# Kernel tuning notes

Measured on AMD Instinct MI355X. Metric: run time of the kernel, lower is better.

Reference implementation:

```python
import jax, jax.numpy as jnp
import numpy as np

T, B, D_IN, D_H, D_MID, D_OUT = 16, 16384, 64, 256, 64, 4


def setup_inputs() -> dict:
    key = jax.random.key(0)
    ks = jax.random.split(key, 12)
    s = 0.05
    return {
        "x": jax.random.normal(ks[0], (T, B, D_IN), dtype=jnp.float32),
        "hc1": jnp.zeros((B, D_H), dtype=jnp.float32),
        "W_i2h": jax.random.normal(ks[1], (D_H, D_IN), dtype=jnp.float32) * s,
        "b_i2h": jax.random.normal(ks[2], (D_H,), dtype=jnp.float32) * s,
        "W_h2h": jax.random.normal(ks[3], (D_H, D_H), dtype=jnp.float32) * s,
        "b_h2h": jax.random.normal(ks[4], (D_H,), dtype=jnp.float32) * s,
        "W_h2o": jax.random.normal(ks[5], (D_MID, D_H), dtype=jnp.float32) * s,
        "b_h2o": jax.random.normal(ks[6], (D_MID,), dtype=jnp.float32) * s,
        "W_fc": jax.random.normal(ks[7], (D_OUT, D_MID), dtype=jnp.float32) * s,
        "b_fc": jax.random.normal(ks[8], (D_OUT,), dtype=jnp.float32) * s,
    }


def reference(x, hc1, W_i2h, b_i2h, W_h2h, b_h2h, W_h2o, b_h2o, W_fc, b_fc):
    # 16-step vanilla RNN: h = tanh(i2h(x_t) + h2h(h)); out = fc(tanh(h2o(h)))
    def step(h, xt):
        h_new = jnp.tanh(xt @ W_i2h.T + b_i2h + h @ W_h2h.T + b_h2h)  # [B, 256]
        out = jnp.tanh(h_new @ W_h2o.T + b_h2o) @ W_fc.T + b_fc       # [B, 4]
        return h_new, out

    h_final, output_seq = jax.lax.scan(step, hc1, x)
    return output_seq, h_final
```

## Files before the change

kernel.cpp:

```cpp
#include <hip/hip_runtime.h>


typedef _Float16 half8 __attribute__((ext_vector_type(8)));
typedef float floatx4 __attribute__((ext_vector_type(4)));

#define T_STEPS 16
#define BATCH   16384
#define HS      264
#define MS      72

__device__ inline float fast_tanh(float x) {
    float t = __builtin_amdgcn_exp2f(x * 2.8853900817779268f);
    return 1.0f - 2.0f * __builtin_amdgcn_rcpf(t + 1.0f);
}

__device__ inline half8 cvt8(const float* __restrict__ p) {
    float4 a = ((const float4*)p)[0];
    float4 b = ((const float4*)p)[1];
    half8 h;
    h[0] = (_Float16)a.x; h[1] = (_Float16)a.y; h[2] = (_Float16)a.z; h[3] = (_Float16)a.w;
    h[4] = (_Float16)b.x; h[5] = (_Float16)b.y; h[6] = (_Float16)b.z; h[7] = (_Float16)b.w;
    return h;
}

__global__ __launch_bounds__(256, 1) void rnn_kernel(
    const float* __restrict__ x,   const float* __restrict__ hc1,
    const float* __restrict__ Wi,  const float* __restrict__ bi,
    const float* __restrict__ Wh,  const float* __restrict__ bh,
    const float* __restrict__ Wo,  const float* __restrict__ bo,
    const float* __restrict__ Wf,  const float* __restrict__ bf,
    float* __restrict__ out)
{
    __shared__ _Float16 h_lds[64 * HS];
    __shared__ _Float16 mid_lds[64 * MS];
    __shared__ float    biasPre[256];
    __shared__ float    bo_lds[64];
    __shared__ _Float16 wfc_lds[4 * 64];
    __shared__ float    bfc_lds[4];

    const int tid  = threadIdx.x;
    const int w    = tid >> 6;
    const int lane = tid & 63;
    const int l16  = lane & 15;
    const int quad = lane >> 4;
    const int b0   = blockIdx.x * 64;

    biasPre[tid] = bi[tid] + bh[tid];
    if (tid < 64) bo_lds[tid] = bo[tid];
    wfc_lds[tid] = (_Float16)Wf[tid];
    if (tid < 4) bfc_lds[tid] = bf[tid];

    {
        int r = tid >> 2, c0 = (tid & 3) * 64;
        const float4* src = (const float4*)&hc1[(size_t)(b0 + r) * 256 + c0];
        #pragma unroll
        for (int i = 0; i < 16; ++i) {
            float4 v = src[i];
            int c = c0 + i * 4;
            h_lds[r * HS + c + 0] = (_Float16)v.x;
            h_lds[r * HS + c + 1] = (_Float16)v.y;
            h_lds[r * HS + c + 2] = (_Float16)v.z;
            h_lds[r * HS + c + 3] = (_Float16)v.w;
        }
    }

    half8 wcat[10][4];
    #pragma unroll
    for (int ks = 0; ks < 10; ++ks) {
        #pragma unroll
        for (int nt = 0; nt < 4; ++nt) {
            int j = w * 64 + nt * 16 + l16;
            const float* src = (ks < 2)
                ? (Wi + (size_t)j * 64  + ks * 32 + quad * 8)
                : (Wh + (size_t)j * 256 + (ks - 2) * 32 + quad * 8);
            wcat[ks][nt] = cvt8(src);
        }
    }
    half8 wof[8];
    #pragma unroll
    for (int ks = 0; ks < 8; ++ks) {
        int j = w * 16 + l16;
        wof[ks] = cvt8(Wo + (size_t)j * 256 + ks * 32 + quad * 8);
    }

    __syncthreads();

    for (int t = 0; t < T_STEPS; ++t) {
        half8 afx[4][2];
        #pragma unroll
        for (int mt = 0; mt < 4; ++mt) {
            int m = mt * 16 + l16;
            const float* xr = x + ((size_t)t * BATCH + b0 + m) * 64;
            #pragma unroll
            for (int k2 = 0; k2 < 2; ++k2)
                afx[mt][k2] = cvt8(xr + k2 * 32 + quad * 8);
        }

        floatx4 acc[4][4];
        #pragma unroll
        for (int mt = 0; mt < 4; ++mt)
            #pragma unroll
            for (int nt = 0; nt < 4; ++nt)
                acc[mt][nt] = (floatx4){0.f, 0.f, 0.f, 0.f};

        #pragma unroll
        for (int ks = 0; ks < 10; ++ks) {
            half8 af[4];
            #pragma unroll
            for (int mt = 0; mt < 4; ++mt) {
                if (ks < 2) {
                    af[mt] = afx[mt][ks];
                } else {
                    int m = mt * 16 + l16;
                    af[mt] = *(const half8*)&h_lds[m * HS + (ks - 2) * 32 + quad * 8];
                }
            }
            #pragma unroll
            for (int mt = 0; mt < 4; ++mt)
                #pragma unroll
                for (int nt = 0; nt < 4; ++nt)
                    acc[mt][nt] = __builtin_amdgcn_mfma_f32_16x16x32_f16(
                        af[mt], wcat[ks][nt], acc[mt][nt], 0, 0, 0);
        }

        __syncthreads();

        #pragma unroll
        for (int nt = 0; nt < 4; ++nt) {
            int col = w * 64 + nt * 16 + l16;
            float bias = biasPre[col];
            #pragma unroll
            for (int mt = 0; mt < 4; ++mt) {
                #pragma unroll
                for (int r = 0; r < 4; ++r) {
                    int row = mt * 16 + quad * 4 + r;
                    h_lds[row * HS + col] = (_Float16)fast_tanh(acc[mt][nt][r] + bias);
                }
            }
        }

        __syncthreads();

        floatx4 acc2[4];
        #pragma unroll
        for (int mt = 0; mt < 4; ++mt) acc2[mt] = (floatx4){0.f, 0.f, 0.f, 0.f};
        #pragma unroll
        for (int ks = 0; ks < 8; ++ks) {
            #pragma unroll
            for (int mt = 0; mt < 4; ++mt) {
                int m = mt * 16 + l16;
                half8 af = *(const half8*)&h_lds[m * HS + ks * 32 + quad * 8];
                acc2[mt] = __builtin_amdgcn_mfma_f32_16x16x32_f16(
                    af, wof[ks], acc2[mt], 0, 0, 0);
            }
        }
        {
            int col = w * 16 + l16;
            float bias = bo_lds[col];
            #pragma unroll
            for (int mt = 0; mt < 4; ++mt)
                #pragma unroll
                for (int r = 0; r < 4; ++r) {
                    int row = mt * 16 + quad * 4 + r;
                    mid_lds[row * MS + col] = (_Float16)fast_tanh(acc2[mt][r] + bias);
                }
        }

        __syncthreads();

        {
            int row = tid >> 2, oc = tid & 3;
            float s = bfc_lds[oc];
            #pragma unroll
            for (int k8 = 0; k8 < 64; k8 += 8) {
                half8 mv = *(const half8*)&mid_lds[row * MS + k8];
                half8 wv = *(const half8*)&wfc_lds[oc * 64 + k8];
                #pragma unroll
                for (int j = 0; j < 8; ++j)
                    s += (float)mv[j] * (float)wv[j];
            }
            out[((size_t)t * BATCH + b0 + row) * 4 + oc] = s;
        }
    }

    {
        int r = tid >> 2, c0 = (tid & 3) * 64;
        float4* dst = (float4*)&out[(size_t)T_STEPS * BATCH * 4 + (size_t)(b0 + r) * 256 + c0];
        #pragma unroll
        for (int i = 0; i < 16; ++i) {
            int c = c0 + i * 4;
            float4 v;
            v.x = (float)h_lds[r * HS + c + 0];
            v.y = (float)h_lds[r * HS + c + 1];
            v.z = (float)h_lds[r * HS + c + 2];
            v.w = (float)h_lds[r * HS + c + 3];
            dst[i] = v;
        }
    }
}

extern "C" void kernel_launch(void* const* d_in, const int* in_sizes, int n_in,
                              void* d_out, int out_size, void* d_ws, size_t ws_size,
                              hipStream_t stream) {
    const float* x   = (const float*)d_in[0];
    const float* hc1 = (const float*)d_in[1];
    const float* Wi  = (const float*)d_in[2];
    const float* bi  = (const float*)d_in[3];
    const float* Wh  = (const float*)d_in[4];
    const float* bh  = (const float*)d_in[5];
    const float* Wo  = (const float*)d_in[6];
    const float* bo  = (const float*)d_in[7];
    const float* Wf  = (const float*)d_in[8];
    const float* bf  = (const float*)d_in[9];

    rnn_kernel<<<256, 256, 0, stream>>>(x, hc1, Wi, bi, Wh, bh, Wo, bo, Wf, bf,
                                        (float*)d_out);
}
```

Baseline: 251.4 us.

## Keep hidden state in registers per wave, swap operands, stream W_h2h from LDS

Restructures the kernel so each wave owns 16 batch rows and computes a transposed product (weights as the A operand, hidden state as the B operand). The hidden state stays in registers across steps and is re-laid out with ds_bpermute instead of LDS round-trips and block-wide barriers. W_h2h is staged once into LDS in MFMA fragment order, the final fc layer also runs on MFMA, biases seed the accumulators, and the next step's x is prefetched. This removes per-step __syncthreads and h LDS traffic, at the cost of 128KB LDS weight reads each step and higher register pressure.

```diff
diff --git a/kernel.cpp b/kernel.cpp
--- a/kernel.cpp
+++ b/kernel.cpp
@@ -3,24 +3,44 @@
 
 typedef _Float16 half8 __attribute__((ext_vector_type(8)));
 typedef float floatx4 __attribute__((ext_vector_type(4)));
+typedef int int4v __attribute__((ext_vector_type(4)));
 
 #define T_STEPS 16
 #define BATCH   16384
-#define HS      264
-#define MS      72
+
+#define MFMA(a,b,c) __builtin_amdgcn_mfma_f32_16x16x32_f16((a),(b),(c),0,0,0)
 
 __device__ inline float fast_tanh(float x) {
     float t = __builtin_amdgcn_exp2f(x * 2.8853900817779268f);
     return 1.0f - 2.0f * __builtin_amdgcn_rcpf(t + 1.0f);
 }
 
-__device__ inline half8 cvt8(const float* __restrict__ p) {
-    float4 a = ((const float4*)p)[0];
-    float4 b = ((const float4*)p)[1];
+__device__ inline half8 cvt8pair(float4 a, float4 b) {
     half8 h;
     h[0] = (_Float16)a.x; h[1] = (_Float16)a.y; h[2] = (_Float16)a.z; h[3] = (_Float16)a.w;
     h[4] = (_Float16)b.x; h[5] = (_Float16)b.y; h[6] = (_Float16)b.z; h[7] = (_Float16)b.w;
     return h;
+}
+
+__device__ inline int pack2h(float a, float b) {
+    _Float16 ha = (_Float16)a, hb = (_Float16)b;
+    unsigned short ua = __builtin_bit_cast(unsigned short, ha);
+    unsigned short ub = __builtin_bit_cast(unsigned short, hb);
+    return (int)ua | ((int)ub << 16);
+}
+
+__device__ inline half8 gatherB(int pkL0, int pkL1, int pkH0, int pkH1,
+                                int addr_lo, int addr_hi, bool hiM) {
+    int a0 = __builtin_amdgcn_ds_bpermute(addr_lo, pkL0);
+    int a1 = __builtin_amdgcn_ds_bpermute(addr_lo, pkL1);
+    int a2 = __builtin_amdgcn_ds_bpermute(addr_hi, pkL0);
+    int a3 = __builtin_amdgcn_ds_bpermute(addr_hi, pkL1);
+    int b0 = __builtin_amdgcn_ds_bpermute(addr_lo, pkH0);
+    int b1 = __builtin_amdgcn_ds_bpermute(addr_lo, pkH1);
+    int b2 = __builtin_amdgcn_ds_bpermute(addr_hi, pkH0);
+    int b3 = __builtin_amdgcn_ds_bpermute(addr_hi, pkH1);
+    int4v v = { hiM ? b0 : a0, hiM ? b1 : a1, hiM ? b2 : a2, hiM ? b3 : a3 };
+    return __builtin_bit_cast(half8, v);
 }
 
 __global__ __launch_bounds__(256, 1) void rnn_kernel(
@@ -28,173 +48,156 @@
     const float* __restrict__ Wi,  const float* __restrict__ bi,
     const float* __restrict__ Wh,  const float* __restrict__ bh,
     const float* __restrict__ Wo,  const float* __restrict__ bo,
-    const float* __restrict__ Wf,  const float* __restrict__ bf,
+    const float* __restrict__ Wf,  const float* __restrict__ bfc,
     float* __restrict__ out)
 {
-    __shared__ _Float16 h_lds[64 * HS];
-    __shared__ _Float16 mid_lds[64 * MS];
-    __shared__ float    biasPre[256];
-    __shared__ float    bo_lds[64];
-    __shared__ _Float16 wfc_lds[4 * 64];
-    __shared__ float    bfc_lds[4];
+    __shared__ _Float16 wh_lds[65536];
+    __shared__ float bpre_l[256];
+    __shared__ float bo_l[64];
 
     const int tid  = threadIdx.x;
     const int w    = tid >> 6;
     const int lane = tid & 63;
     const int l16  = lane & 15;
     const int quad = lane >> 4;
-    const int b0   = blockIdx.x * 64;
-
-    biasPre[tid] = bi[tid] + bh[tid];
-    if (tid < 64) bo_lds[tid] = bo[tid];
-    wfc_lds[tid] = (_Float16)Wf[tid];
-    if (tid < 4) bfc_lds[tid] = bf[tid];
-
+    const int myrow = blockIdx.x * 64 + w * 16 + l16;
+
+    bpre_l[tid] = bi[tid] + bh[tid];
+    if (tid < 64) bo_l[tid] = bo[tid];
+
+    #pragma unroll
+    for (int i = 0; i < 32; ++i) {
+        int u = tid + 256 * i;
+        int c = u >> 6, lu = u & 63;
+        int row = (c >> 3) * 16 + (lu & 15);
+        int col = (c & 7) * 32 + (lu >> 4) * 8;
+        const float4* s = (const float4*)&Wh[row * 256 + col];
+        *(half8*)&wh_lds[u * 8] = cvt8pair(s[0], s[1]);
+    }
+
+    half8 wiA[16][2];
+    #pragma unroll
+    for (int M = 0; M < 16; ++M)
+        #pragma unroll
+        for (int kt = 0; kt < 2; ++kt) {
+            const float4* s = (const float4*)&Wi[(M * 16 + l16) * 64 + kt * 32 + quad * 8];
+            wiA[M][kt] = cvt8pair(s[0], s[1]);
+        }
+    half8 woA[4][8];
+    #pragma unroll
+    for (int M2 = 0; M2 < 4; ++M2)
+        #pragma unroll
+        for (int ks = 0; ks < 8; ++ks) {
+            const float4* s = (const float4*)&Wo[(M2 * 16 + l16) * 256 + ks * 32 + quad * 8];
+            woA[M2][ks] = cvt8pair(s[0], s[1]);
+        }
+    half8 wfA[2];
+    #pragma unroll
+    for (int kt = 0; kt < 2; ++kt) {
+        half8 z = (half8){0,0,0,0,0,0,0,0};
+        if (l16 < 4) {
+            const float4* s = (const float4*)&Wf[l16 * 64 + kt * 32 + quad * 8];
+            z = cvt8pair(s[0], s[1]);
+        }
+        wfA[kt] = z;
+    }
+    const float4 bfcv = *(const float4*)bfc;
+
+    half8 hB[8];
+    #pragma unroll
+    for (int ks = 0; ks < 8; ++ks) {
+        const float4* s = (const float4*)&hc1[(size_t)myrow * 256 + ks * 32 + quad * 8];
+        hB[ks] = cvt8pair(s[0], s[1]);
+    }
+    half8 xB[2];
     {
-        int r = tid >> 2, c0 = (tid & 3) * 64;
-        const float4* src = (const float4*)&hc1[(size_t)(b0 + r) * 256 + c0];
-        #pragma unroll
-        for (int i = 0; i < 16; ++i) {
-            float4 v = src[i];
-            int c = c0 + i * 4;
-            h_lds[r * HS + c + 0] = (_Float16)v.x;
-            h_lds[r * HS + c + 1] = (_Float16)v.y;
-            h_lds[r * HS + c + 2] = (_Float16)v.z;
-            h_lds[r * HS + c + 3] = (_Float16)v.w;
-        }
-    }
-
-    half8 wcat[10][4];
-    #pragma unroll
-    for (int ks = 0; ks < 10; ++ks) {
-        #pragma unroll
-        for (int nt = 0; nt < 4; ++nt) {
-            int j = w * 64 + nt * 16 + l16;
-            const float* src = (ks < 2)
-                ? (Wi + (size_t)j * 64  + ks * 32 + quad * 8)
-                : (Wh + (size_t)j * 256 + (ks - 2) * 32 + quad * 8);
-            wcat[ks][nt] = cvt8(src);
-        }
-    }
-    half8 wof[8];
-    #pragma unroll
-    for (int ks = 0; ks < 8; ++ks) {
-        int j = w * 16 + l16;
-        wof[ks] = cvt8(Wo + (size_t)j * 256 + ks * 32 + quad * 8);
-    }
+        const float* xp = x + (size_t)myrow * 64 + quad * 8;
+        xB[0] = cvt8pair(((const float4*)xp)[0], ((const float4*)xp)[1]);
+        xB[1] = cvt8pair(((const float4*)(xp + 32))[0], ((const float4*)(xp + 32))[1]);
+    }
+
+    const int addr_lo = (l16 + 32 * (quad & 1)) * 4;
+    const int addr_hi = addr_lo + 64;
+    const bool hiM = quad >= 2;
 
     __syncthreads();
 
     for (int t = 0; t < T_STEPS; ++t) {
-        half8 afx[4][2];
-        #pragma unroll
-        for (int mt = 0; mt < 4; ++mt) {
-            int m = mt * 16 + l16;
-            const float* xr = x + ((size_t)t * BATCH + b0 + m) * 64;
+        float4 xr0, xr1, xr2, xr3;
+        if (t < T_STEPS - 1) {
+            const float* xp = x + ((size_t)(t + 1) * BATCH + myrow) * 64 + quad * 8;
+            xr0 = ((const float4*)xp)[0];        xr1 = ((const float4*)xp)[1];
+            xr2 = ((const float4*)(xp + 32))[0]; xr3 = ((const float4*)(xp + 32))[1];
+        }
+
+        int pk[16][2];
+        #pragma unroll
+        for (int Mp = 0; Mp < 8; ++Mp) {
+            const int M0 = 2 * Mp, M1 = M0 + 1;
+            floatx4 acc0 = *(const floatx4*)&bpre_l[M0 * 16 + quad * 4];
+            floatx4 acc1 = *(const floatx4*)&bpre_l[M1 * 16 + quad * 4];
+            acc0 = MFMA(wiA[M0][0], xB[0], acc0);
+            acc1 = MFMA(wiA[M1][0], xB[0], acc1);
+            acc0 = MFMA(wiA[M0][1], xB[1], acc0);
+            acc1 = MFMA(wiA[M1][1], xB[1], acc1);
             #pragma unroll
-            for (int k2 = 0; k2 < 2; ++k2)
-                afx[mt][k2] = cvt8(xr + k2 * 32 + quad * 8);
-        }
-
-        floatx4 acc[4][4];
-        #pragma unroll
-        for (int mt = 0; mt < 4; ++mt)
+            for (int ks = 0; ks < 8; ++ks) {
+                half8 a0 = *(const half8*)&wh_lds[((M0 * 8 + ks) * 64 + lane) * 8];
+                half8 a1 = *(const half8*)&wh_lds[((M1 * 8 + ks) * 64 + lane) * 8];
+                acc0 = MFMA(a0, hB[ks], acc0);
+                acc1 = MFMA(a1, hB[ks], acc1);
+            }
+            pk[M0][0] = pack2h(fast_tanh(acc0[0] ), fast_tanh(acc0[1]));
+            pk[M0][1] = pack2h(fast_tanh(acc0[2]), fast_tanh(acc0[3]));
+            pk[M1][0] = pack2h(fast_tanh(acc1[0]), fast_tanh(acc1[1]));
+            pk[M1][1] = pack2h(fast_tanh(acc1[2]), fast_tanh(acc1[3]));
+        }
+        #pragma unroll
+        for (int ks = 0; ks < 8; ++ks)
+            hB[ks] = gatherB(pk[2*ks][0], pk[2*ks][1], pk[2*ks+1][0], pk[2*ks+1][1],
+                             addr_lo, addr_hi, hiM);
+
+        int pkm[4][2];
+        #pragma unroll
+        for (int M2 = 0; M2 < 4; ++M2) {
+            floatx4 m = *(const floatx4*)&bo_l[M2 * 16 + quad * 4];
             #pragma unroll
-            for (int nt = 0; nt < 4; ++nt)
-                acc[mt][nt] = (floatx4){0.f, 0.f, 0.f, 0.f};
-
-        #pragma unroll
-        for (int ks = 0; ks < 10; ++ks) {
-            half8 af[4];
-            #pragma unroll
-            for (int mt = 0; mt < 4; ++mt) {
-                if (ks < 2) {
-                    af[mt] = afx[mt][ks];
-                } else {
-                    int m = mt * 16 + l16;
-                    af[mt] = *(const half8*)&h_lds[m * HS + (ks - 2) * 32 + quad * 8];
-                }
-            }
-            #pragma unroll
-            for (int mt = 0; mt < 4; ++mt)
-                #pragma unroll
-                for (int nt = 0; nt < 4; ++nt)
-                    acc[mt][nt] = __builtin_amdgcn_mfma_f32_16x16x32_f16(
-                        af[mt], wcat[ks][nt], acc[mt][nt], 0, 0, 0);
-        }
-
-        __syncthreads();
-
-        #pragma unroll
-        for (int nt = 0; nt < 4; ++nt) {
-            int col = w * 64 + nt * 16 + l16;
-            float bias = biasPre[col];
-            #pragma unroll
-            for (int mt = 0; mt < 4; ++mt) {
-                #pragma unroll
-                for (int r = 0; r < 4; ++r) {
-                    int row = mt * 16 + quad * 4 + r;
-                    h_lds[row * HS + col] = (_Float16)fast_tanh(acc[mt][nt][r] + bias);
-                }
-            }
-        }
-
-        __syncthreads();
-
-        floatx4 acc2[4];
-        #pragma unroll
-        for (int mt = 0; mt < 4; ++mt) acc2[mt] = (floatx4){0.f, 0.f, 0.f, 0.f};
+            for (int ks = 0; ks < 8; ++ks)
+                m = MFMA(woA[M2][ks], hB[ks], m);
+            pkm[M2][0] = pack2h(fast_tanh(m[0]), fast_tanh(m[1]));
+            pkm[M2][1] = pack2h(fast_tanh(m[2]), fast_tanh(m[3]));
+        }
+        half8 mB0 = gatherB(pkm[0][0], pkm[0][1], pkm[1][0], pkm[1][1],
+                            addr_lo, addr_hi, hiM);
+        half8 mB1 = gatherB(pkm[2][0], pkm[2][1], pkm[3][0], pkm[3][1],
+                            addr_lo, addr_hi, hiM);
+        floatx4 f = {0.f, 0.f, 0.f, 0.f};
+        f = MFMA(wfA[0], mB0, f);
+        f = MFMA(wfA[1], mB1, f);
+        if (quad == 0) {
+            float4 o;
+            o.x = f[0] + bfcv.x; o.y = f[1] + bfcv.y;
+            o.z = f[2] + bfcv.z; o.w = f[3] + bfcv.w;
+            *(float4*)&out[((size_t)t * BATCH + myrow) * 4] = o;
+        }
+
+        if (t < T_STEPS - 1) {
+            xB[0] = cvt8pair(xr0, xr1);
+            xB[1] = cvt8pair(xr2, xr3);
+        }
+    }
+
+    {
+        float* hf = out + (size_t)T_STEPS * BATCH * 4 + (size_t)myrow * 256;
         #pragma unroll
         for (int ks = 0; ks < 8; ++ks) {
-            #pragma unroll
-            for (int mt = 0; mt < 4; ++mt) {
-                int m = mt * 16 + l16;
-                half8 af = *(const half8*)&h_lds[m * HS + ks * 32 + quad * 8];
-                acc2[mt] = __builtin_amdgcn_mfma_f32_16x16x32_f16(
-                    af, wof[ks], acc2[mt], 0, 0, 0);
-            }
-        }
-        {
-            int col = w * 16 + l16;
-            float bias = bo_lds[col];
-            #pragma unroll
-            for (int mt = 0; mt < 4; ++mt)
-                #pragma unroll
-                for (int r = 0; r < 4; ++r) {
-                    int row = mt * 16 + quad * 4 + r;
-                    mid_lds[row * MS + col] = (_Float16)fast_tanh(acc2[mt][r] + bias);
-                }
-        }
-
-        __syncthreads();
-
-        {
-            int row = tid >> 2, oc = tid & 3;
-            float s = bfc_lds[oc];
-            #pragma unroll
-            for (int k8 = 0; k8 < 64; k8 += 8) {
-                half8 mv = *(const half8*)&mid_lds[row * MS + k8];
-                half8 wv = *(const half8*)&wfc_lds[oc * 64 + k8];
-                #pragma unroll
-                for (int j = 0; j < 8; ++j)
-                    s += (float)mv[j] * (float)wv[j];
-            }
-            out[((size_t)t * BATCH + b0 + row) * 4 + oc] = s;
-        }
-    }
-
-    {
-        int r = tid >> 2, c0 = (tid & 3) * 64;
-        float4* dst = (float4*)&out[(size_t)T_STEPS * BATCH * 4 + (size_t)(b0 + r) * 256 + c0];
-        #pragma unroll
-        for (int i = 0; i < 16; ++i) {
-            int c = c0 + i * 4;
-            float4 v;
-            v.x = (float)h_lds[r * HS + c + 0];
-            v.y = (float)h_lds[r * HS + c + 1];
-            v.z = (float)h_lds[r * HS + c + 2];
-            v.w = (float)h_lds[r * HS + c + 3];
-            dst[i] = v;
+            float4 o0, o1;
+            o0.x = (float)hB[ks][0]; o0.y = (float)hB[ks][1];
+            o0.z = (float)hB[ks][2]; o0.w = (float)hB[ks][3];
+            o1.x = (float)hB[ks][4]; o1.y = (float)hB[ks][5];
+            o1.z = (float)hB[ks][6]; o1.w = (float)hB[ks][7];
+            *(float4*)&hf[ks * 32 + quad * 8]     = o0;
+            *(float4*)&hf[ks * 32 + quad * 8 + 4] = o1;
         }
     }
 }
```

Result: slower. 690.6 us (+174.7%).
